# Kernel tuning notes

Measured on AMD Instinct MI355X. Metric: run time of the kernel, lower is better.

Reference implementation:

```python
import jax, jax.numpy as jnp
import numpy as np
from jax import lax

B, N, K = 8, 4096, 16          # clouds, points per cloud, knn neighbors
RATIO = 0.5
M = int(N * RATIO)             # sampled points per cloud (fps ratio)
C_IN, C_OUT = 64, 128
EPS = 1e-5                      # BatchNorm eps


def setup_inputs() -> dict:
    key = jax.random.key(0)
    ks = jax.random.split(key, 4)
    x = jax.random.normal(ks[0], (B * N, C_IN), jnp.float32)
    pos = jax.random.uniform(ks[1], (B * N, 3), jnp.float32)
    batch = jnp.repeat(jnp.arange(B, dtype=jnp.int32), N)
    W = jax.random.normal(ks[2], (C_IN, C_OUT), jnp.float32) / np.sqrt(C_IN).astype(np.float32)
    b = jnp.zeros((C_OUT,), jnp.float32)
    gamma = jnp.ones((C_OUT,), jnp.float32)
    beta = jnp.zeros((C_OUT,), jnp.float32)
    return {"x": x, "pos": pos, "batch": batch, "W": W, "b": b, "gamma": gamma, "beta": beta}


def _fps(pos_c):
    # Farthest point sampling on one cloud. pos_c: [N,3] -> [M] local indices.
    # Deterministic start at index 0 (reference for torch_cluster.fps).
    def step(carry, _):
        dmin, last = carry
        d = jnp.sum((pos_c - pos_c[last]) ** 2, axis=-1)   # [N]
        dmin = jnp.minimum(dmin, d)
        nxt = jnp.argmax(dmin).astype(jnp.int32)
        return (dmin, nxt), last
    init = (jnp.full((pos_c.shape[0],), jnp.inf, pos_c.dtype), jnp.int32(0))
    _, idx = lax.scan(step, init, None, length=M)
    return idx


def _knn(pos_c, qpos_c):
    # k nearest original points for each sampled point. [N,3],[M,3] -> [M,K].
    d = jnp.sum((qpos_c[:, None, :] - pos_c[None, :, :]) ** 2, axis=-1)  # [M,N]
    _, idx = lax.top_k(-d, K)
    return idx


def reference(x, pos, batch, W, b, gamma, beta):
    pos_b = pos.reshape(B, N, 3)
    fps_idx = jax.vmap(_fps)(pos_b)                                       # [B,M]
    new_pos_b = jnp.take_along_axis(pos_b, fps_idx[:, :, None], axis=1)   # [B,M,3]
    nbr = jax.vmap(_knn)(pos_b, new_pos_b)                                # [B,M,K]

    # mlp: Linear -> BatchNorm1d (training-mode batch stats) -> GELU
    h = x @ W + b                                                         # [B*N,C_OUT]
    mu = jnp.mean(h, axis=0)
    var = jnp.mean((h - mu) ** 2, axis=0)
    h = (h - mu) * lax.rsqrt(var + EPS) * gamma + beta
    h = jax.nn.gelu(h, approximate=False)
    h_b = h.reshape(B, N, C_OUT)

    # gather neighbor features; scatter-max over edge_index[0] == max over K
    # (each sampled point has exactly K incoming edges)
    feats = jax.vmap(lambda hb, nb: hb[nb])(h_b, nbr)                     # [B,M,K,C_OUT]
    new_x = jnp.max(feats, axis=2).reshape(B * M, C_OUT)
    new_pos = new_pos_b.reshape(B * M, 3)
    new_batch = jnp.repeat(jnp.arange(B, dtype=batch.dtype), M)
    return (new_x, new_pos, new_batch)
```

## Files before the change

kernel.cpp:

```cpp
#include <hip/hip_runtime.h>
#include <math.h>

#define NB 8
#define NN 4096
#define MM 2048
#define KNN_K 16
#define CIN 64
#define COUT 128
#define BN_EPS 1e-5f
#define FPS_THR 512
#define PTS 8

typedef float v2f __attribute__((ext_vector_type(2)));

__device__ __forceinline__ v2f pk_add(v2f a, v2f b) {
  v2f r;
  asm("v_pk_add_f32 %0, %1, %2" : "=v"(r) : "v"(a), "v"(b));
  return r;
}
__device__ __forceinline__ v2f pk_mul(v2f a, v2f b) {
  v2f r;
  asm("v_pk_mul_f32 %0, %1, %2" : "=v"(r) : "v"(a), "v"(b));
  return r;
}

__device__ __forceinline__ double pack_key(float d, unsigned code) {
  return __longlong_as_double(
      (long long)(((unsigned long long)__float_as_uint(d) << 32) | code));
}
__device__ __forceinline__ unsigned unpack_code(double v) {
  return (unsigned)((unsigned long long)__double_as_longlong(v) &
                    0xFFFFFFFFull);
}

__device__ __forceinline__ float sqdist_np(float dx, float dy, float dz) {
  return __fadd_rn(__fadd_rn(__fmul_rn(dx, dx), __fmul_rn(dy, dy)),
                   __fmul_rn(dz, dz));
}

#define DPP_MAX_LEVEL(best, ctrl, rmask)                                     \
  {                                                                          \
    const int _lo = __builtin_amdgcn_update_dpp(                             \
        __double2loint(best), __double2loint(best), (ctrl), (rmask), 0xf,    \
        false);                                                              \
    const int _hi = __builtin_amdgcn_update_dpp(                             \
        __double2hiint(best), __double2hiint(best), (ctrl), (rmask), 0xf,    \
        false);                                                              \
    best = fmax(best, __hiloint2double(_hi, _lo));                           \
  }

__global__ __launch_bounds__(512) void k_fps_gemm(
    const float* __restrict__ pos, const float* __restrict__ x,
    const float* __restrict__ W, const float* __restrict__ bias,
    float* __restrict__ h, float* __restrict__ gsum,
    float* __restrict__ gsumsq, int* __restrict__ fps_idx,
    float* __restrict__ out_pos, float* __restrict__ out_batch) {
  __shared__ __align__(16) char smem_raw[73856];
  const int tid = threadIdx.x;

  if (blockIdx.x < NB) {
    float* pos4 = (float*)smem_raw;
    int* idxs = (int*)(smem_raw + 65536);
    double* red = (double*)(smem_raw + 73728);
    const int b = blockIdx.x;
    const float* posc = pos + (size_t)b * NN * 3;
    for (int p = tid; p < NN; p += FPS_THR) {
      pos4[4 * p + 0] = posc[3 * p + 0];
      pos4[4 * p + 1] = posc[3 * p + 1];
      pos4[4 * p + 2] = posc[3 * p + 2];
    }
    if (tid == 0) idxs[0] = 0;

    v2f pxv[4], pyv[4], pzv[4];
    float dmin[PTS];
    const int p0 = tid * PTS;
    const unsigned code_base = (unsigned)(NN - 1 - p0);
#pragma unroll
    for (int u = 0; u < 4; ++u) {
      const int p = p0 + 2 * u;
      pxv[u] = (v2f){posc[3 * p + 0], posc[3 * p + 3]};
      pyv[u] = (v2f){posc[3 * p + 1], posc[3 * p + 4]};
      pzv[u] = (v2f){posc[3 * p + 2], posc[3 * p + 5]};
      dmin[2 * u] = __int_as_float(0x7f800000);
      dmin[2 * u + 1] = __int_as_float(0x7f800000);
    }
    __syncthreads();
    const int lane = tid & 63, wv = tid >> 6;
    float lx = pos4[0], ly = pos4[1], lz = pos4[2];
    for (int m = 1; m < MM; ++m) {
      const v2f nlx = {-lx, -lx}, nly = {-ly, -ly}, nlz = {-lz, -lz};
#pragma unroll
      for (int u = 0; u < 4; ++u) {
        const v2f dx = pk_add(pxv[u], nlx);
        const v2f dy = pk_add(pyv[u], nly);
        const v2f dz = pk_add(pzv[u], nlz);
        const v2f d2 =
            pk_add(pk_add(pk_mul(dx, dx), pk_mul(dy, dy)), pk_mul(dz, dz));
        dmin[2 * u] = fminf(dmin[2 * u], d2.x);
        dmin[2 * u + 1] = fminf(dmin[2 * u + 1], d2.y);
      }
      const float M =
          fmaxf(fmaxf(fmaxf(fmaxf(dmin[0], dmin[1]), fmaxf(dmin[2], dmin[3])),
                      fmaxf(dmin[4], dmin[5])),
                fmaxf(dmin[6], dmin[7]));
      unsigned sel = code_base - 7;
#pragma unroll
      for (int s = 6; s >= 0; --s)
        sel = (dmin[s] == M) ? (code_base - s) : sel;
      double best = pack_key(M, sel);
      DPP_MAX_LEVEL(best, 0x121, 0xf);
      DPP_MAX_LEVEL(best, 0x122, 0xf);
      DPP_MAX_LEVEL(best, 0x124, 0xf);
      DPP_MAX_LEVEL(best, 0x128, 0xf);
      DPP_MAX_LEVEL(best, 0x142, 0xa);
      DPP_MAX_LEVEL(best, 0x143, 0xc);
      const int par = (m & 1) * 8;
      if (lane == 63) red[par + wv] = best;
      __syncthreads();
      const double2* rp = (const double2*)&red[par];
      const double2 r0 = rp[0], r1 = rp[1], r2 = rp[2], r3 = rp[3];
      const double f =
          fmax(fmax(fmax(r0.x, r0.y), fmax(r1.x, r1.y)),
               fmax(fmax(r2.x, r2.y), fmax(r3.x, r3.y)));
      const int last = (NN - 1) - (int)unpack_code(f);
      if (tid == 0) idxs[m] = last;
      const float4 lp = *(const float4*)&pos4[4 * last];
      lx = lp.x;
      ly = lp.y;
      lz = lp.z;
    }
    __syncthreads();
    for (int m = tid; m < MM; m += FPS_THR) {
      const int p = idxs[m];
      const int o = b * MM + m;
      const float4 pp = *(const float4*)&pos4[4 * p];
      fps_idx[o] = p;
      out_pos[o * 3 + 0] = pp.x;
      out_pos[o * 3 + 1] = pp.y;
      out_pos[o * 3 + 2] = pp.z;
      out_batch[o] = (float)b;
    }
  } else {
    float* Wl = (float*)smem_raw;
    float* xl = Wl + CIN * COUT;
    float* bsum = (float*)(smem_raw + 49152);
    float* bsq = bsum + COUT;
    const int bid = blockIdx.x - NB;
    const int r0 = bid * 64;
    for (int i = tid; i < CIN * COUT; i += FPS_THR) Wl[i] = W[i];
    for (int i = tid; i < 64 * CIN; i += FPS_THR)
      xl[i] = x[(size_t)r0 * CIN + i];
    if (tid < 2 * COUT) ((float*)(smem_raw + 49152))[tid] = 0.f;
    __syncthreads();
    const int cg = tid & 31, rg = tid >> 5;
    const int c = cg * 4;
    float acc[4][4];
#pragma unroll
    for (int j = 0; j < 4; ++j)
#pragma unroll
      for (int t = 0; t < 4; ++t) acc[j][t] = 0.f;
    for (int k = 0; k < CIN; ++k) {
      const float4 wk = *(const float4*)&Wl[k * COUT + c];
#pragma unroll
      for (int j = 0; j < 4; ++j) {
        const float xv = xl[(rg * 4 + j) * CIN + k];
        acc[j][0] = fmaf(xv, wk.x, acc[j][0]);
        acc[j][1] = fmaf(xv, wk.y, acc[j][1]);
        acc[j][2] = fmaf(xv, wk.z, acc[j][2]);
        acc[j][3] = fmaf(xv, wk.w, acc[j][3]);
      }
    }
    const float4 bb = *(const float4*)&bias[c];
    float s0 = 0, s1 = 0, s2 = 0, s3 = 0, q0 = 0, q1 = 0, q2 = 0, q3 = 0;
#pragma unroll
    for (int j = 0; j < 4; ++j) {
      float4 hv;
      hv.x = acc[j][0] + bb.x;
      hv.y = acc[j][1] + bb.y;
      hv.z = acc[j][2] + bb.z;
      hv.w = acc[j][3] + bb.w;
      *(float4*)&h[(size_t)(r0 + rg * 4 + j) * COUT + c] = hv;
      s0 += hv.x; s1 += hv.y; s2 += hv.z; s3 += hv.w;
      q0 += hv.x * hv.x; q1 += hv.y * hv.y;
      q2 += hv.z * hv.z; q3 += hv.w * hv.w;
    }
    atomicAdd(&bsum[c + 0], s0); atomicAdd(&bsum[c + 1], s1);
    atomicAdd(&bsum[c + 2], s2); atomicAdd(&bsum[c + 3], s3);
    atomicAdd(&bsq[c + 0], q0);  atomicAdd(&bsq[c + 1], q1);
    atomicAdd(&bsq[c + 2], q2);  atomicAdd(&bsq[c + 3], q3);
    __syncthreads();
    if (tid < COUT) {
      atomicAdd(&gsum[tid], bsum[tid]);
      atomicAdd(&gsumsq[tid], bsq[tid]);
    }
  }
}

__device__ __forceinline__ float gelu_exact(float v) {
  return 0.5f * v * (1.0f + erff(v * 0.70710678118654752f));
}

__global__ __launch_bounds__(256) void k_act(float* __restrict__ h,
                                             const float* __restrict__ gsum,
                                             const float* __restrict__ gsumsq,
                                             const float* __restrict__ gamma,
                                             const float* __restrict__ beta) {
  __shared__ float sc[COUT], sh[COUT];
  const int t = threadIdx.x;
  if (t < COUT) {
    const float n = (float)(NB * NN);
    const float mu = gsum[t] / n;
    const float var = gsumsq[t] / n - mu * mu;
    const float rs = rsqrtf(var + BN_EPS);
    const float s = rs * gamma[t];
    sc[t] = s;
    sh[t] = beta[t] - mu * s;
  }
  __syncthreads();
  const int g = blockIdx.x * 256 + t;
  const int c = (g & 31) * 4;
  float4* h4 = (float4*)h;
  float4 v = h4[g];
  const float4 s4 = *(const float4*)&sc[c];
  const float4 b4 = *(const float4*)&sh[c];
  v.x = gelu_exact(v.x * s4.x + b4.x);
  v.y = gelu_exact(v.y * s4.y + b4.y);
  v.z = gelu_exact(v.z * s4.z + b4.z);
  v.w = gelu_exact(v.w * s4.w + b4.w);
  h4[g] = v;
}

__global__ __launch_bounds__(256) void k_knn(const float* __restrict__ pos,
                                             const int* __restrict__ fps_idx,
                                             const float* __restrict__ h,
                                             float* __restrict__ out_x) {
  __shared__ float dc[4][NN];
  const int tid = threadIdx.x, lane = tid & 63, wv = tid >> 6;
  const int q = blockIdx.x * 4 + wv;
  const int b = q >> 11, m = q & (MM - 1);
  const int qi = fps_idx[b * MM + m];
  const float* posc = pos + (size_t)b * NN * 3;
  const float qx = posc[qi * 3 + 0], qy = posc[qi * 3 + 1],
              qz = posc[qi * 3 + 2];
  float* dcw = dc[wv];
  const double DINF = __longlong_as_double(0x7FF0000000000000LL);
  double gmin[8];
#pragma unroll
  for (int g = 0; g < 8; ++g) gmin[g] = DINF;
#pragma unroll
  for (int s = 0; s < 64; ++s) {
    const int p = s * 64 + lane;
    const float d = sqdist_np(posc[p * 3 + 0] - qx, posc[p * 3 + 1] - qy,
                              posc[p * 3 + 2] - qz);
    dcw[p] = d;
    gmin[s >> 3] = fmin(gmin[s >> 3], pack_key(d, (unsigned)p));
  }
  double lmin = gmin[0];
#pragma unroll
  for (int g = 1; g < 8; ++g) lmin = fmin(lmin, gmin[g]);

  int nbr[KNN_K];
#pragma unroll
  for (int r = 0; r < KNN_K; ++r) {
    double v = lmin;
#pragma unroll
    for (int off = 32; off; off >>= 1) v = fmin(v, __shfl_xor(v, off, 64));
    const unsigned p = unpack_code(v);
    nbr[r] = (int)p;
    if (lane == (int)(p & 63)) {
      dcw[p] = __int_as_float(0x7f800000);
      const int g = (int)(p >> 9);
      double nm = DINF;
      const int base = g * 8 * 64 + lane;
#pragma unroll
      for (int j = 0; j < 8; ++j) {
        const int pp = base + j * 64;
        nm = fmin(nm, pack_key(dcw[pp], (unsigned)pp));
      }
#pragma unroll
      for (int gg = 0; gg < 8; ++gg)
        if (gg == g) gmin[gg] = nm;
      lmin = gmin[0];
#pragma unroll
      for (int gg = 1; gg < 8; ++gg) lmin = fmin(lmin, gmin[gg]);
    }
  }

  const float* hb = h + (size_t)b * NN * COUT;
  float f0 = -__int_as_float(0x7f800000), f1 = f0;
#pragma unroll
  for (int r = 0; r < KNN_K; ++r) {
    const float* row = hb + (size_t)nbr[r] * COUT;
    f0 = fmaxf(f0, row[lane]);
    f1 = fmaxf(f1, row[lane + 64]);
  }
  out_x[(size_t)q * COUT + lane] = f0;
  out_x[(size_t)q * COUT + lane + 64] = f1;
}

extern "C" void kernel_launch(void* const* d_in, const int* in_sizes, int n_in,
                              void* d_out, int out_size, void* d_ws,
                              size_t ws_size, hipStream_t stream) {
  const float* x = (const float*)d_in[0];
  const float* pos = (const float*)d_in[1];
  const float* W = (const float*)d_in[3];
  const float* bias = (const float*)d_in[4];
  const float* gamma = (const float*)d_in[5];
  const float* beta = (const float*)d_in[6];

  float* out_x = (float*)d_out;
  float* out_pos = out_x + (size_t)NB * MM * COUT;
  float* out_batch = out_pos + (size_t)NB * MM * 3;

  char* ws = (char*)d_ws;
  float* h = (float*)ws;
  float* gsum = (float*)(ws + (size_t)16777216);
  float* gsumsq = gsum + COUT;
  int* fps_idx = (int*)(gsumsq + COUT);

  (void)hipMemsetAsync(gsum, 0, 2 * COUT * sizeof(float), stream);
  hipLaunchKernelGGL(k_fps_gemm, dim3(NB + 512), dim3(FPS_THR), 0, stream, pos,
                     x, W, bias, h, gsum, gsumsq, fps_idx, out_pos, out_batch);
  hipLaunchKernelGGL(k_act, dim3(4096), dim3(256), 0, stream, h, gsum, gsumsq,
                     gamma, beta);
  hipLaunchKernelGGL(k_knn, dim3(4096), dim3(256), 0, stream, pos, fps_idx, h,
                     out_x);
}
```

Measured before the change: 1.428 ms.

## Fuse BN+GELU into kNN gather, shrink FPS block to 256, DPP wave min

Drops the separate activation kernel: the kNN kernel now computes the BatchNorm scale and shift per block and applies BN+GELU to each gathered neighbour row before the max. FPS blocks shrink from 512 to 256 threads with 16 points per thread, halving the cross-wave reduction, and the GEMM side computes 8 rows per thread. The kNN argmin uses DPP row ops plus a readlane instead of xor shuffles. In exchange, GELU/erf is evaluated 16 times per output (about 4M rows x 128) instead of once per h element (32K rows), and the serial FPS loop does more per-thread work per iteration.

```diff
diff --git a/kernel.cpp b/kernel.cpp
--- a/kernel.cpp
+++ b/kernel.cpp
@@ -8,8 +8,6 @@
 #define CIN 64
 #define COUT 128
 #define BN_EPS 1e-5f
-#define FPS_THR 512
-#define PTS 8
 
 typedef float v2f __attribute__((ext_vector_type(2)));
 
@@ -48,8 +46,18 @@
         false);                                                              \
     best = fmax(best, __hiloint2double(_hi, _lo));                           \
   }
-
-__global__ __launch_bounds__(512) void k_fps_gemm(
+#define DPP_MIN_LEVEL(best, ctrl, rmask)                                     \
+  {                                                                          \
+    const int _lo = __builtin_amdgcn_update_dpp(                             \
+        __double2loint(best), __double2loint(best), (ctrl), (rmask), 0xf,    \
+        false);                                                              \
+    const int _hi = __builtin_amdgcn_update_dpp(                             \
+        __double2hiint(best), __double2hiint(best), (ctrl), (rmask), 0xf,    \
+        false);                                                              \
+    best = fmin(best, __hiloint2double(_hi, _lo));                           \
+  }
+
+__global__ __launch_bounds__(256) void k_fps_gemm(
     const float* __restrict__ pos, const float* __restrict__ x,
     const float* __restrict__ W, const float* __restrict__ bias,
     float* __restrict__ h, float* __restrict__ gsum,
@@ -64,19 +72,19 @@
     double* red = (double*)(smem_raw + 73728);
     const int b = blockIdx.x;
     const float* posc = pos + (size_t)b * NN * 3;
-    for (int p = tid; p < NN; p += FPS_THR) {
+    for (int p = tid; p < NN; p += 256) {
       pos4[4 * p + 0] = posc[3 * p + 0];
       pos4[4 * p + 1] = posc[3 * p + 1];
       pos4[4 * p + 2] = posc[3 * p + 2];
     }
     if (tid == 0) idxs[0] = 0;
 
-    v2f pxv[4], pyv[4], pzv[4];
-    float dmin[PTS];
-    const int p0 = tid * PTS;
+    v2f pxv[8], pyv[8], pzv[8];
+    float dmin[16];
+    const int p0 = tid * 16;
     const unsigned code_base = (unsigned)(NN - 1 - p0);
 #pragma unroll
-    for (int u = 0; u < 4; ++u) {
+    for (int u = 0; u < 8; ++u) {
       const int p = p0 + 2 * u;
       pxv[u] = (v2f){posc[3 * p + 0], posc[3 * p + 3]};
       pyv[u] = (v2f){posc[3 * p + 1], posc[3 * p + 4]};
@@ -90,7 +98,7 @@
     for (int m = 1; m < MM; ++m) {
       const v2f nlx = {-lx, -lx}, nly = {-ly, -ly}, nlz = {-lz, -lz};
 #pragma unroll
-      for (int u = 0; u < 4; ++u) {
+      for (int u = 0; u < 8; ++u) {
         const v2f dx = pk_add(pxv[u], nlx);
         const v2f dy = pk_add(pyv[u], nly);
         const v2f dz = pk_add(pzv[u], nlz);
@@ -99,13 +107,12 @@
         dmin[2 * u] = fminf(dmin[2 * u], d2.x);
         dmin[2 * u + 1] = fminf(dmin[2 * u + 1], d2.y);
       }
-      const float M =
-          fmaxf(fmaxf(fmaxf(fmaxf(dmin[0], dmin[1]), fmaxf(dmin[2], dmin[3])),
-                      fmaxf(dmin[4], dmin[5])),
-                fmaxf(dmin[6], dmin[7]));
-      unsigned sel = code_base - 7;
-#pragma unroll
-      for (int s = 6; s >= 0; --s)
+      float M = fmaxf(dmin[0], dmin[1]);
+#pragma unroll
+      for (int s = 2; s < 16; ++s) M = fmaxf(M, dmin[s]);
+      unsigned sel = code_base - 15;
+#pragma unroll
+      for (int s = 14; s >= 0; --s)
         sel = (dmin[s] == M) ? (code_base - s) : sel;
       double best = pack_key(M, sel);
       DPP_MAX_LEVEL(best, 0x121, 0xf);
@@ -114,14 +121,12 @@
       DPP_MAX_LEVEL(best, 0x128, 0xf);
       DPP_MAX_LEVEL(best, 0x142, 0xa);
       DPP_MAX_LEVEL(best, 0x143, 0xc);
-      const int par = (m & 1) * 8;
+      const int par = (m & 1) * 4;
       if (lane == 63) red[par + wv] = best;
       __syncthreads();
       const double2* rp = (const double2*)&red[par];
-      const double2 r0 = rp[0], r1 = rp[1], r2 = rp[2], r3 = rp[3];
-      const double f =
-          fmax(fmax(fmax(r0.x, r0.y), fmax(r1.x, r1.y)),
-               fmax(fmax(r2.x, r2.y), fmax(r3.x, r3.y)));
+      const double2 r0 = rp[0], r1 = rp[1];
+      const double f = fmax(fmax(r0.x, r0.y), fmax(r1.x, r1.y));
       const int last = (NN - 1) - (int)unpack_code(f);
       if (tid == 0) idxs[m] = last;
       const float4 lp = *(const float4*)&pos4[4 * last];
@@ -130,7 +135,7 @@
       lz = lp.z;
     }
     __syncthreads();
-    for (int m = tid; m < MM; m += FPS_THR) {
+    for (int m = tid; m < MM; m += 256) {
       const int p = idxs[m];
       const int o = b * MM + m;
       const float4 pp = *(const float4*)&pos4[4 * p];
@@ -147,23 +152,22 @@
     float* bsq = bsum + COUT;
     const int bid = blockIdx.x - NB;
     const int r0 = bid * 64;
-    for (int i = tid; i < CIN * COUT; i += FPS_THR) Wl[i] = W[i];
-    for (int i = tid; i < 64 * CIN; i += FPS_THR)
-      xl[i] = x[(size_t)r0 * CIN + i];
-    if (tid < 2 * COUT) ((float*)(smem_raw + 49152))[tid] = 0.f;
+    for (int i = tid; i < CIN * COUT; i += 256) Wl[i] = W[i];
+    for (int i = tid; i < 64 * CIN; i += 256) xl[i] = x[(size_t)r0 * CIN + i];
+    if (tid < 2 * COUT) bsum[tid] = 0.f;
     __syncthreads();
     const int cg = tid & 31, rg = tid >> 5;
     const int c = cg * 4;
-    float acc[4][4];
-#pragma unroll
-    for (int j = 0; j < 4; ++j)
+    float acc[8][4];
+#pragma unroll
+    for (int j = 0; j < 8; ++j)
 #pragma unroll
       for (int t = 0; t < 4; ++t) acc[j][t] = 0.f;
     for (int k = 0; k < CIN; ++k) {
       const float4 wk = *(const float4*)&Wl[k * COUT + c];
 #pragma unroll
-      for (int j = 0; j < 4; ++j) {
-        const float xv = xl[(rg * 4 + j) * CIN + k];
+      for (int j = 0; j < 8; ++j) {
+        const float xv = xl[(rg * 8 + j) * CIN + k];
         acc[j][0] = fmaf(xv, wk.x, acc[j][0]);
         acc[j][1] = fmaf(xv, wk.y, acc[j][1]);
         acc[j][2] = fmaf(xv, wk.z, acc[j][2]);
@@ -173,13 +177,13 @@
     const float4 bb = *(const float4*)&bias[c];
     float s0 = 0, s1 = 0, s2 = 0, s3 = 0, q0 = 0, q1 = 0, q2 = 0, q3 = 0;
 #pragma unroll
-    for (int j = 0; j < 4; ++j) {
+    for (int j = 0; j < 8; ++j) {
       float4 hv;
       hv.x = acc[j][0] + bb.x;
       hv.y = acc[j][1] + bb.y;
       hv.z = acc[j][2] + bb.z;
       hv.w = acc[j][3] + bb.w;
-      *(float4*)&h[(size_t)(r0 + rg * 4 + j) * COUT + c] = hv;
+      *(float4*)&h[(size_t)(r0 + rg * 8 + j) * COUT + c] = hv;
       s0 += hv.x; s1 += hv.y; s2 += hv.z; s3 += hv.w;
       q0 += hv.x * hv.x; q1 += hv.y * hv.y;
       q2 += hv.z * hv.z; q3 += hv.w * hv.w;
@@ -200,42 +204,24 @@
   return 0.5f * v * (1.0f + erff(v * 0.70710678118654752f));
 }
 
-__global__ __launch_bounds__(256) void k_act(float* __restrict__ h,
-                                             const float* __restrict__ gsum,
-                                             const float* __restrict__ gsumsq,
-                                             const float* __restrict__ gamma,
-                                             const float* __restrict__ beta) {
+__global__ __launch_bounds__(256) void k_knn(
+    const float* __restrict__ pos, const int* __restrict__ fps_idx,
+    const float* __restrict__ h, const float* __restrict__ gsum,
+    const float* __restrict__ gsumsq, const float* __restrict__ gamma,
+    const float* __restrict__ beta, float* __restrict__ out_x) {
+  __shared__ float dc[4][NN];
   __shared__ float sc[COUT], sh[COUT];
-  const int t = threadIdx.x;
-  if (t < COUT) {
+  const int tid = threadIdx.x, lane = tid & 63, wv = tid >> 6;
+  if (tid < COUT) {
     const float n = (float)(NB * NN);
-    const float mu = gsum[t] / n;
-    const float var = gsumsq[t] / n - mu * mu;
+    const float mu = gsum[tid] / n;
+    const float var = gsumsq[tid] / n - mu * mu;
     const float rs = rsqrtf(var + BN_EPS);
-    const float s = rs * gamma[t];
-    sc[t] = s;
-    sh[t] = beta[t] - mu * s;
+    const float s = rs * gamma[tid];
+    sc[tid] = s;
+    sh[tid] = beta[tid] - mu * s;
   }
   __syncthreads();
-  const int g = blockIdx.x * 256 + t;
-  const int c = (g & 31) * 4;
-  float4* h4 = (float4*)h;
-  float4 v = h4[g];
-  const float4 s4 = *(const float4*)&sc[c];
-  const float4 b4 = *(const float4*)&sh[c];
-  v.x = gelu_exact(v.x * s4.x + b4.x);
-  v.y = gelu_exact(v.y * s4.y + b4.y);
-  v.z = gelu_exact(v.z * s4.z + b4.z);
-  v.w = gelu_exact(v.w * s4.w + b4.w);
-  h4[g] = v;
-}
-
-__global__ __launch_bounds__(256) void k_knn(const float* __restrict__ pos,
-                                             const int* __restrict__ fps_idx,
-                                             const float* __restrict__ h,
-                                             float* __restrict__ out_x) {
-  __shared__ float dc[4][NN];
-  const int tid = threadIdx.x, lane = tid & 63, wv = tid >> 6;
   const int q = blockIdx.x * 4 + wv;
   const int b = q >> 11, m = q & (MM - 1);
   const int qi = fps_idx[b * MM + m];
@@ -263,9 +249,14 @@
 #pragma unroll
   for (int r = 0; r < KNN_K; ++r) {
     double v = lmin;
-#pragma unroll
-    for (int off = 32; off; off >>= 1) v = fmin(v, __shfl_xor(v, off, 64));
-    const unsigned p = unpack_code(v);
+    DPP_MIN_LEVEL(v, 0x121, 0xf);
+    DPP_MIN_LEVEL(v, 0x122, 0xf);
+    DPP_MIN_LEVEL(v, 0x124, 0xf);
+    DPP_MIN_LEVEL(v, 0x128, 0xf);
+    DPP_MIN_LEVEL(v, 0x142, 0xa);
+    DPP_MIN_LEVEL(v, 0x143, 0xc);
+    const unsigned p =
+        (unsigned)__builtin_amdgcn_readlane(__double2loint(v), 63);
     nbr[r] = (int)p;
     if (lane == (int)(p & 63)) {
       dcw[p] = __int_as_float(0x7f800000);
@@ -287,12 +278,14 @@
   }
 
   const float* hb = h + (size_t)b * NN * COUT;
+  const float sc0 = sc[lane], sh0 = sh[lane];
+  const float sc1 = sc[lane + 64], sh1 = sh[lane + 64];
   float f0 = -__int_as_float(0x7f800000), f1 = f0;
 #pragma unroll
   for (int r = 0; r < KNN_K; ++r) {
     const float* row = hb + (size_t)nbr[r] * COUT;
-    f0 = fmaxf(f0, row[lane]);
-    f1 = fmaxf(f1, row[lane + 64]);
+    f0 = fmaxf(f0, gelu_exact(fmaf(row[lane], sc0, sh0)));
+    f1 = fmaxf(f1, gelu_exact(fmaf(row[lane + 64], sc1, sh1)));
   }
   out_x[(size_t)q * COUT + lane] = f0;
   out_x[(size_t)q * COUT + lane + 64] = f1;
@@ -319,10 +312,8 @@
   int* fps_idx = (int*)(gsumsq + COUT);
 
   (void)hipMemsetAsync(gsum, 0, 2 * COUT * sizeof(float), stream);
-  hipLaunchKernelGGL(k_fps_gemm, dim3(NB + 512), dim3(FPS_THR), 0, stream, pos,
-                     x, W, bias, h, gsum, gsumsq, fps_idx, out_pos, out_batch);
-  hipLaunchKernelGGL(k_act, dim3(4096), dim3(256), 0, stream, h, gsum, gsumsq,
-                     gamma, beta);
+  hipLaunchKernelGGL(k_fps_gemm, dim3(NB + 512), dim3(256), 0, stream, pos, x,
+                     W, bias, h, gsum, gsumsq, fps_idx, out_pos, out_batch);
   hipLaunchKernelGGL(k_knn, dim3(4096), dim3(256), 0, stream, pos, fps_idx, h,
-                     out_x);
-}
+                     gsum, gsumsq, gamma, beta, out_x);
+}
```

Result: no change. 1.411 ms (-1.2%).
